# Performance work log

Hardware: AMD Instinct MI355X
Metric: run time of the kernel (lower is better)

Reference implementation:

```python
import jax, jax.numpy as jnp
import numpy as np

D_MODEL = 1024
N_HEADS = 16
D_K = D_MODEL // N_HEADS
D_FF = 4096
B, S = 4, 2048
EPS = 1e-5


def setup_inputs() -> dict:
    key = jax.random.key(0)
    ks = jax.random.split(key, 16)
    s = 0.02
    inp = {
        'x': jax.random.normal(ks[0], (B, S, D_MODEL), dtype=jnp.float32),
        'Wq': jax.random.normal(ks[1], (D_MODEL, D_MODEL), dtype=jnp.float32) * s,
        'bq': jnp.zeros((D_MODEL,), jnp.float32),
        'Wk': jax.random.normal(ks[2], (D_MODEL, D_MODEL), dtype=jnp.float32) * s,
        'bk': jnp.zeros((D_MODEL,), jnp.float32),
        'Wv': jax.random.normal(ks[3], (D_MODEL, D_MODEL), dtype=jnp.float32) * s,
        'bv': jnp.zeros((D_MODEL,), jnp.float32),
        'Wo': jax.random.normal(ks[4], (D_MODEL, D_MODEL), dtype=jnp.float32) * s,
        'bo': jnp.zeros((D_MODEL,), jnp.float32),
        'W1': jax.random.normal(ks[5], (D_MODEL, D_FF), dtype=jnp.float32) * s,
        'b1': jnp.zeros((D_FF,), jnp.float32),
        'W2': jax.random.normal(ks[6], (D_FF, D_MODEL), dtype=jnp.float32) * s,
        'b2': jnp.zeros((D_MODEL,), jnp.float32),
        'g1': jnp.ones((D_MODEL,), jnp.float32),
        'be1': jnp.zeros((D_MODEL,), jnp.float32),
        'g2': jnp.ones((D_MODEL,), jnp.float32),
        'be2': jnp.zeros((D_MODEL,), jnp.float32),
    }
    return inp


def _layernorm(x, g, b):
    mu = jnp.mean(x, axis=-1, keepdims=True)
    var = jnp.var(x, axis=-1, keepdims=True)
    return (x - mu) * jax.lax.rsqrt(var + EPS) * g + b


def reference(x, Wq, bq, Wk, bk, Wv, bv, Wo, bo, W1, b1, W2, b2, g1, be1, g2, be2):
    # Multi-head self-attention (mask=None, dropout in eval -> identity)
    q = (x @ Wq + bq).reshape(B, S, N_HEADS, D_K).transpose(0, 2, 1, 3)  # [B,H,S,Dk]
    k = (x @ Wk + bk).reshape(B, S, N_HEADS, D_K).transpose(0, 2, 1, 3)
    v = (x @ Wv + bv).reshape(B, S, N_HEADS, D_K).transpose(0, 2, 1, 3)
    scores = jnp.einsum('bhqd,bhkd->bhqk', q, k) / jnp.sqrt(jnp.float32(D_K))
    attn = jax.nn.softmax(scores, axis=-1)
    out = jnp.einsum('bhqk,bhkd->bhqd', attn, v)          # [B,H,S,Dk]
    out = out.transpose(0, 2, 1, 3).reshape(B, S, D_MODEL)
    att_out = out @ Wo + bo
    x2 = _layernorm(x + att_out, g1, be1)
    ff = jax.nn.relu(x2 @ W1 + b1) @ W2 + b2
    return _layernorm(x2 + ff, g2, be2)
```

## Files before the change

### kernel.cpp

```cpp
#include <hip/hip_runtime.h>
#include <hip/hip_bf16.h>

typedef __attribute__((ext_vector_type(8)))  __bf16 bf16x8;
typedef __attribute__((ext_vector_type(4)))  float  f32x4;
typedef __attribute__((ext_vector_type(16))) float  f32x16;

static __device__ __forceinline__ unsigned short f2bf(float x) {
    unsigned int u = __float_as_uint(x);
    unsigned int r = (u + 0x7FFFu + ((u >> 16) & 1u)) >> 16;
    return (unsigned short)r;
}
static __device__ __forceinline__ float bf2f(unsigned short u) {
    return __uint_as_float(((unsigned int)u) << 16);
}

static __device__ __forceinline__ float fast_exp2(float x) {
    float r;
    asm("v_exp_f32 %0, %1" : "=v"(r) : "v"(x));
    return r;
}
static __device__ __forceinline__ unsigned int cvt_pk_bf16(float a, float b) {
    unsigned int r;
    asm("v_cvt_pk_bf16_f32 %0, %1, %2" : "=v"(r) : "v"(a), "v"(b));
    return r;
}

static __device__ __forceinline__ void gload_lds16(const ushort* g, ushort* l) {
    __builtin_amdgcn_global_load_lds((const __attribute__((address_space(1))) void*)g,
                                     (__attribute__((address_space(3))) void*)l, 16, 0, 0);
}

static __device__ __forceinline__ void barrier_fence() {
    __builtin_amdgcn_s_barrier();
    __builtin_amdgcn_sched_barrier(0);
    asm volatile("" ::: "memory");
}

static __device__ __forceinline__ int xcd_swz(int id, int nwg) {
    return (id & 7) * (nwg >> 3) + (id >> 3);
}

__global__ __launch_bounds__(256) void cast_bf16_kernel(const float* __restrict__ in,
                                                        ushort* __restrict__ out, int n4) {
    int i = blockIdx.x * 256 + threadIdx.x;
    if (i < n4) {
        float4 v = reinterpret_cast<const float4*>(in)[i];
        ushort4 o;
        o.x = f2bf(v.x); o.y = f2bf(v.y); o.z = f2bf(v.z); o.w = f2bf(v.w);
        reinterpret_cast<ushort4*>(out)[i] = o;
    }
}

__global__ __launch_bounds__(256) void transpose_cast_kernel(const float* __restrict__ in,
                                                             ushort* __restrict__ out,
                                                             int K, int N) {
    __shared__ float tile[32][33];
    const int tx = threadIdx.x;
    const int ty = threadIdx.y;
    const int n0 = blockIdx.x * 32;
    const int k0 = blockIdx.y * 32;
    for (int i = ty; i < 32; i += 8)
        tile[i][tx] = in[(size_t)(k0 + i) * N + n0 + tx];
    __syncthreads();
    for (int i = ty; i < 32; i += 8)
        out[(size_t)(n0 + i) * K + k0 + tx] = f2bf(tile[tx][i]);
}

__global__ __launch_bounds__(256) void transpose_cast3_kernel(const float* __restrict__ w0,
                                                              const float* __restrict__ w1,
                                                              const float* __restrict__ w2,
                                                              ushort* __restrict__ out) {
    __shared__ float tile[32][33];
    const int tx = threadIdx.x;
    const int ty = threadIdx.y;
    const int n0 = blockIdx.x * 32;
    const int k0 = blockIdx.y * 32;
    const int z  = blockIdx.z;
    const float* in = (z == 0) ? w0 : (z == 1 ? w1 : w2);
    ushort* o = out + (size_t)z * 1024 * 1024;
    for (int i = ty; i < 32; i += 8)
        tile[i][tx] = in[(size_t)(k0 + i) * 1024 + n0 + tx];
    __syncthreads();
    for (int i = ty; i < 32; i += 8)
        o[(size_t)(n0 + i) * 1024 + k0 + tx] = f2bf(tile[tx][i]);
}

template<int RELU, int OUTBF, int QKV, int RES>
__global__ __launch_bounds__(256) void gemm_p3(const ushort* __restrict__ A,
                                               const ushort* __restrict__ Bt,
                                               const float* __restrict__ b0,
                                               const float* __restrict__ b1_,
                                               const float* __restrict__ b2_,
                                               const void* __restrict__ xres,
                                               void* __restrict__ Cp,
                                               int M, int N, int K) {
    __shared__ ushort As[3][4096];
    __shared__ ushort Bs[3][4096];
    const int tid  = threadIdx.x;
    const int lane = tid & 63;
    const int w    = tid >> 6;
    const int wr   = w >> 1, wc = w & 1;
    const int nwg = gridDim.x * gridDim.y;
    int wid = xcd_swz(blockIdx.y * gridDim.x + blockIdx.x, nwg);
    const int bx = wid % gridDim.x;
    const int by = wid / gridDim.x;
    const int m0 = by * 128;
    const int n0 = bx * 128;
    const int lr = lane & 15;
    const int lg = lane >> 4;
    const int xc = (lg ^ ((lr >> 1) & 3)) * 8;

    const int r0 = w * 32 + (lane >> 2);
    const int c8 = ((lane & 3) ^ ((lane >> 3) & 3)) * 8;
    const ushort* gA0 = A  + (size_t)(m0 + r0)      * K + c8;
    const ushort* gA1 = A  + (size_t)(m0 + r0 + 16) * K + c8;
    const ushort* gB0 = Bt + (size_t)(n0 + r0)      * K + c8;
    const ushort* gB1 = Bt + (size_t)(n0 + r0 + 16) * K + c8;
    const int wb = w * 1024;

    f32x4 acc[4][4];
    const f32x4 z = {0.f, 0.f, 0.f, 0.f};
#pragma unroll
    for (int i = 0; i < 4; i++)
#pragma unroll
        for (int j = 0; j < 4; j++) acc[i][j] = z;

    const int nt = K >> 5;

#pragma unroll
    for (int t = 0; t < 2; ++t) {
        const int kn = t * 32;
        gload_lds16(gA0 + kn, &As[t][wb]);
        gload_lds16(gA1 + kn, &As[t][wb + 512]);
        gload_lds16(gB0 + kn, &Bs[t][wb]);
        gload_lds16(gB1 + kn, &Bs[t][wb + 512]);
    }

    int cur = 0;
    for (int t = 0; t < nt; ++t) {
        if (t + 1 < nt) asm volatile("s_waitcnt vmcnt(4)" ::: "memory");
        else            asm volatile("s_waitcnt vmcnt(0)" ::: "memory");
        barrier_fence();

        if (t + 2 < nt) {
            const int bi = (cur + 2 >= 3) ? cur - 1 : cur + 2;
            const int kn = (t + 2) * 32;
            gload_lds16(gA0 + kn, &As[bi][wb]);
            gload_lds16(gA1 + kn, &As[bi][wb + 512]);
            gload_lds16(gB0 + kn, &Bs[bi][wb]);
            gload_lds16(gB1 + kn, &Bs[bi][wb + 512]);
        }

        const ushort* Asb = As[cur];
        const ushort* Bsb = Bs[cur];
        bf16x8 af[4], bfr[4];
#pragma unroll
        for (int i = 0; i < 4; i++)
            af[i] = *reinterpret_cast<const bf16x8*>(&Asb[(wr * 64 + i * 16 + lr) * 32 + xc]);
#pragma unroll
        for (int j = 0; j < 4; j++)
            bfr[j] = *reinterpret_cast<const bf16x8*>(&Bsb[(wc * 64 + j * 16 + lr) * 32 + xc]);
#pragma unroll
        for (int i = 0; i < 4; i++)
#pragma unroll
            for (int j = 0; j < 4; j++)
                acc[i][j] = __builtin_amdgcn_mfma_f32_16x16x32_bf16(af[i], bfr[j], acc[i][j], 0, 0, 0);

        cur = (cur == 2) ? 0 : cur + 1;
    }

    const float* bias;
    float qscale = 1.0f;
    if (QKV) {
        bias = (n0 < 1024) ? b0 : (n0 < 2048 ? b1_ : b2_);
        if (n0 < 1024) qscale = 0.18033688f;
    } else {
        bias = b0;
    }
    const int nb = QKV ? (n0 & 1023) : n0;
    const int rbase = (lane >> 4) * 4;
#pragma unroll
    for (int i = 0; i < 4; i++) {
#pragma unroll
        for (int j = 0; j < 4; j++) {
            const int cloc = wc * 64 + j * 16 + lr;
            const float bv = bias[nb + cloc];
#pragma unroll
            for (int r = 0; r < 4; r++) {
                const int row = m0 + wr * 64 + i * 16 + rbase + r;
                float v = acc[i][j][r] + bv;
                if (RES == 1) v += ((const float*)xres)[(size_t)row * N + n0 + cloc];
                if (RES == 2) v += bf2f(((const ushort*)xres)[(size_t)row * N + n0 + cloc]);
                if (RELU) v = v > 0.f ? v : 0.f;
                if (QKV)  v *= qscale;
                if (OUTBF) ((ushort*)Cp)[(size_t)row * N + n0 + cloc] = f2bf(v);
                else       ((float*)Cp)[(size_t)row * N + n0 + cloc] = v;
            }
        }
    }
}

template<int RELU, int OUTBF, int RES>
__global__ __launch_bounds__(256) void gemm_n64(const ushort* __restrict__ A,
                                                const ushort* __restrict__ Bt,
                                                const float* __restrict__ bias,
                                                const void* __restrict__ xres,
                                                void* __restrict__ Cp,
                                                int M, int N, int K) {
    __shared__ ushort As[3][4096];
    __shared__ ushort Bs[3][2048];
    const int tid  = threadIdx.x;
    const int lane = tid & 63;
    const int w    = tid >> 6;
    const int wr   = w >> 1, wc = w & 1;
    const int nwg = gridDim.x * gridDim.y;
    int wid = xcd_swz(blockIdx.y * gridDim.x + blockIdx.x, nwg);
    const int bx = wid % gridDim.x;
    const int by = wid / gridDim.x;
    const int m0 = by * 128;
    const int n0 = bx * 64;
    const int lr = lane & 15;
    const int lg = lane >> 4;
    const int xc = (lg ^ ((lr >> 1) & 3)) * 8;

    const int r0 = w * 32 + (lane >> 2);
    const int c8 = ((lane & 3) ^ ((lane >> 3) & 3)) * 8;
    const ushort* gA0 = A  + (size_t)(m0 + r0)      * K + c8;
    const ushort* gA1 = A  + (size_t)(m0 + r0 + 16) * K + c8;
    const ushort* gB0 = Bt + (size_t)(n0 + (tid >> 2)) * K + c8;
    const int wb  = w * 1024;
    const int wbB = w * 512;

    f32x4 acc[4][2];
    const f32x4 z = {0.f, 0.f, 0.f, 0.f};
#pragma unroll
    for (int i = 0; i < 4; i++)
#pragma unroll
        for (int j = 0; j < 2; j++) acc[i][j] = z;

    const int nt = K >> 5;

#pragma unroll
    for (int t = 0; t < 2; ++t) {
        const int kn = t * 32;
        gload_lds16(gA0 + kn, &As[t][wb]);
        gload_lds16(gA1 + kn, &As[t][wb + 512]);
        gload_lds16(gB0 + kn, &Bs[t][wbB]);
    }

    int cur = 0;
    for (int t = 0; t < nt; ++t) {
        if (t + 1 < nt) asm volatile("s_waitcnt vmcnt(3)" ::: "memory");
        else            asm volatile("s_waitcnt vmcnt(0)" ::: "memory");
        barrier_fence();

        if (t + 2 < nt) {
            const int bi = (cur + 2 >= 3) ? cur - 1 : cur + 2;
            const int kn = (t + 2) * 32;
            gload_lds16(gA0 + kn, &As[bi][wb]);
            gload_lds16(gA1 + kn, &As[bi][wb + 512]);
            gload_lds16(gB0 + kn, &Bs[bi][wbB]);
        }

        const ushort* Asb = As[cur];
        const ushort* Bsb = Bs[cur];
        bf16x8 af[4], bfr[2];
#pragma unroll
        for (int i = 0; i < 4; i++)
            af[i] = *reinterpret_cast<const bf16x8*>(&Asb[(wr * 64 + i * 16 + lr) * 32 + xc]);
#pragma unroll
        for (int j = 0; j < 2; j++)
            bfr[j] = *reinterpret_cast<const bf16x8*>(&Bsb[(wc * 32 + j * 16 + lr) * 32 + xc]);
#pragma unroll
        for (int i = 0; i < 4; i++)
#pragma unroll
            for (int j = 0; j < 2; j++)
                acc[i][j] = __builtin_amdgcn_mfma_f32_16x16x32_bf16(af[i], bfr[j], acc[i][j], 0, 0, 0);

        cur = (cur == 2) ? 0 : cur + 1;
    }

    const int rbase = (lane >> 4) * 4;
#pragma unroll
    for (int i = 0; i < 4; i++) {
#pragma unroll
        for (int j = 0; j < 2; j++) {
            const int cloc = wc * 32 + j * 16 + lr;
            const float bv = bias[n0 + cloc];
#pragma unroll
            for (int r = 0; r < 4; r++) {
                const int row = m0 + wr * 64 + i * 16 + rbase + r;
                float v = acc[i][j][r] + bv;
                if (RES == 1) v += ((const float*)xres)[(size_t)row * N + n0 + cloc];
                if (RES == 2) v += bf2f(((const ushort*)xres)[(size_t)row * N + n0 + cloc]);
                if (RELU) v = v > 0.f ? v : 0.f;
                if (OUTBF) ((ushort*)Cp)[(size_t)row * N + n0 + cloc] = f2bf(v);
                else       ((float*)Cp)[(size_t)row * N + n0 + cloc] = v;
            }
        }
    }
}

#define ASWZ(row, col) ((row) * 64 + ((col) ^ ((((row) ^ ((row) >> 3)) & 7) << 3)))

__global__ __launch_bounds__(256, 3) void attn_kernel(const ushort* __restrict__ QKV,
                                                      ushort* __restrict__ O) {
    __shared__ ushort Ks[2][4096];
    __shared__ ushort Vt[2][4096];
    const int tid  = threadIdx.x;
    const int lane = tid & 63;
    const int w    = tid >> 6;
    const int l31  = lane & 31;
    const int hi   = lane >> 5;

    int blk = xcd_swz(blockIdx.x, gridDim.x);
    const int qb = blk & 15;
    const int h  = (blk >> 4) & 15;
    const int b  = blk >> 8;
    const int s0 = qb * 128 + w * 32;
    const size_t rowb   = (size_t)b * 2048;
    const size_t base_q = rowb * 3072 + (size_t)h * 64;
    const size_t base_k = base_q + 1024;
    const size_t base_v = base_q + 2048;
    const size_t base_o = rowb * 1024 + (size_t)h * 64;

    bf16x8 qf[4];
#pragma unroll
    for (int ks = 0; ks < 4; ks++)
        qf[ks] = *reinterpret_cast<const bf16x8*>(
            &QKV[base_q + (size_t)(s0 + l31) * 3072 + ks * 16 + 8 * hi]);

    int off8[2][4];
#pragma unroll
    for (int sub = 0; sub < 2; sub++)
#pragma unroll
        for (int ks = 0; ks < 4; ks++)
            off8[sub][ks] = ASWZ(sub * 32 + l31, ks * 16 + 8 * hi);

    const int tS2 = tid >> 3;
    const int ccS = tid & 7;
    int voff[8];
#pragma unroll
    for (int jj = 0; jj < 8; jj++)
        voff[jj] = ASWZ(ccS * 8 + jj, 2 * tS2);
    const int tk1 = tS2 + 32;
    const int sz0 = (tS2 ^ (tS2 >> 3)) & 7;
    const int sz1 = (tk1 ^ (tk1 >> 3)) & 7;
    const ushort* pK0 = QKV + base_k + (size_t)tS2 * 3072 + (ccS ^ sz0) * 8;
    const ushort* pK1 = QKV + base_k + (size_t)tk1 * 3072 + (ccS ^ sz1) * 8;
    const ushort* pV0 = QKV + base_v + (size_t)(2 * tS2)     * 3072 + ccS * 8;
    const ushort* pV1 = QKV + base_v + (size_t)(2 * tS2 + 1) * 3072 + ccS * 8;
    const size_t step = (size_t)64 * 3072;

    gload_lds16(pK0, &Ks[0][w * 512]);
    gload_lds16(pK1, &Ks[0][2048 + w * 512]);
    {
        int4 v0 = *reinterpret_cast<const int4*>(pV0);
        int4 v1 = *reinterpret_cast<const int4*>(pV1);
        const ushort* vs0 = reinterpret_cast<const ushort*>(&v0);
        const ushort* vs1 = reinterpret_cast<const ushort*>(&v1);
#pragma unroll
        for (int jj = 0; jj < 8; jj++)
            *reinterpret_cast<unsigned*>(&Vt[0][voff[jj]]) =
                (unsigned)vs0[jj] | ((unsigned)vs1[jj] << 16);
    }
    pK0 += step; pK1 += step; pV0 += step; pV1 += step;
    __syncthreads();

    f32x16 oacc0, oacc1;
    for (int i = 0; i < 16; i++) { oacc0[i] = 0.f; oacc1[i] = 0.f; }
    float lacc = 0.f;
    int cur = 0;

    for (int it = 0; it < 32; ++it) {
        int4 nv0, nv1;
        if (it < 31) {
            gload_lds16(pK0, &Ks[cur ^ 1][w * 512]);
            gload_lds16(pK1, &Ks[cur ^ 1][2048 + w * 512]);
            nv0 = *reinterpret_cast<const int4*>(pV0);
            nv1 = *reinterpret_cast<const int4*>(pV1);
            pK0 += step; pK1 += step; pV0 += step; pV1 += step;
        }

        f32x16 sa0, sa1;
        for (int i = 0; i < 16; i++) { sa0[i] = 0.f; sa1[i] = 0.f; }
        __builtin_amdgcn_s_setprio(1);
#pragma unroll
        for (int ks = 0; ks < 4; ks++) {
            bf16x8 k0 = *reinterpret_cast<const bf16x8*>(&Ks[cur][off8[0][ks]]);
            sa0 = __builtin_amdgcn_mfma_f32_32x32x16_bf16(k0, qf[ks], sa0, 0, 0, 0);
        }
#pragma unroll
        for (int ks = 0; ks < 4; ks++) {
            bf16x8 k1 = *reinterpret_cast<const bf16x8*>(&Ks[cur][off8[1][ks]]);
            sa1 = __builtin_amdgcn_mfma_f32_32x32x16_bf16(k1, qf[ks], sa1, 0, 0, 0);
        }
        __builtin_amdgcn_s_setprio(0);

        unsigned pk0[8], pk1[8];
#pragma unroll
        for (int i = 0; i < 8; i++) {
            float plo = fast_exp2(sa0[2 * i]);
            float phi = fast_exp2(sa0[2 * i + 1]);
            lacc += plo + phi;
            pk0[i] = cvt_pk_bf16(plo, phi);
        }
#pragma unroll
        for (int i = 0; i < 8; i++) {
            float plo = fast_exp2(sa1[2 * i]);
            float phi = fast_exp2(sa1[2 * i + 1]);
            lacc += plo + phi;
            pk1[i] = cvt_pk_bf16(plo, phi);
        }

        __builtin_amdgcn_s_setprio(1);
#pragma unroll
        for (int ks = 0; ks < 4; ks++) {
            const int bi = 4 * (ks & 1);
            unsigned a, bb, c, d;
            if (ks < 2) { a = pk0[bi]; bb = pk0[bi + 1]; c = pk0[bi + 2]; d = pk0[bi + 3]; }
            else        { a = pk1[bi]; bb = pk1[bi + 1]; c = pk1[bi + 2]; d = pk1[bi + 3]; }
            asm("v_permlane32_swap_b32 %0, %1" : "+v"(a), "+v"(c));
            asm("v_permlane32_swap_b32 %0, %1" : "+v"(bb), "+v"(d));
            union { unsigned u[4]; bf16x8 v; } fr;
            fr.u[0] = a; fr.u[1] = bb; fr.u[2] = c; fr.u[3] = d;
            bf16x8 v0 = *reinterpret_cast<const bf16x8*>(&Vt[cur][off8[0][ks]]);
            oacc0 = __builtin_amdgcn_mfma_f32_32x32x16_bf16(fr.v, v0, oacc0, 0, 0, 0);
            bf16x8 v1 = *reinterpret_cast<const bf16x8*>(&Vt[cur][off8[1][ks]]);
            oacc1 = __builtin_amdgcn_mfma_f32_32x32x16_bf16(fr.v, v1, oacc1, 0, 0, 0);
        }
        __builtin_amdgcn_s_setprio(0);

        if (it < 31) {
            const ushort* vs0 = reinterpret_cast<const ushort*>(&nv0);
            const ushort* vs1 = reinterpret_cast<const ushort*>(&nv1);
#pragma unroll
            for (int jj = 0; jj < 8; jj++)
                *reinterpret_cast<unsigned*>(&Vt[cur ^ 1][voff[jj]]) =
                    (unsigned)vs0[jj] | ((unsigned)vs1[jj] << 16);
        }
        __syncthreads();
        cur ^= 1;
    }

    const float ltot = lacc + __shfl_xor(lacc, 32);
    const float inv  = 1.f / ltot;
#pragma unroll
    for (int r = 0; r < 16; r++) {
        const int qloc = (r & 3) + 8 * (r >> 2) + 4 * hi;
        const float invq = __shfl(inv, qloc);
        const size_t rowoff = base_o + (size_t)(s0 + qloc) * 1024 + l31;
        O[rowoff]      = f2bf(oacc0[r] * invq);
        O[rowoff + 32] = f2bf(oacc1[r] * invq);
    }
}

template<int OUTBF>
__global__ __launch_bounds__(256) void ln_one(const ushort* __restrict__ zin,
                                              const float* __restrict__ g,
                                              const float* __restrict__ be,
                                              void* __restrict__ out) {
    const int row = blockIdx.x;
    const int tid = threadIdx.x;
    const ushort4 zv = reinterpret_cast<const ushort4*>(zin + (size_t)row * 1024)[tid];
    float v[4] = {bf2f(zv.x), bf2f(zv.y), bf2f(zv.z), bf2f(zv.w)};
    float s  = v[0] + v[1] + v[2] + v[3];
    float s2 = v[0]*v[0] + v[1]*v[1] + v[2]*v[2] + v[3]*v[3];
    for (int off = 32; off; off >>= 1) { s += __shfl_down(s, off); s2 += __shfl_down(s2, off); }
    __shared__ float red[8];
    const int w = tid >> 6, lane = tid & 63;
    if (lane == 0) { red[w] = s; red[4 + w] = s2; }
    __syncthreads();
    if (tid == 0) {
        const float ts  = red[0] + red[1] + red[2] + red[3];
        const float ts2 = red[4] + red[5] + red[6] + red[7];
        const float mu  = ts * (1.f / 1024.f);
        const float var = ts2 * (1.f / 1024.f) - mu * mu;
        red[0] = mu;
        red[1] = rsqrtf(var + 1e-5f);
    }
    __syncthreads();
    const float mu = red[0], rs = red[1];
    const float4 gv = reinterpret_cast<const float4*>(g)[tid];
    const float4 bv = reinterpret_cast<const float4*>(be)[tid];
    float o0 = (v[0] - mu) * rs * gv.x + bv.x;
    float o1 = (v[1] - mu) * rs * gv.y + bv.y;
    float o2 = (v[2] - mu) * rs * gv.z + bv.z;
    float o3 = (v[3] - mu) * rs * gv.w + bv.w;
    if (OUTBF) {
        ushort4 ob;
        ob.x = f2bf(o0); ob.y = f2bf(o1); ob.z = f2bf(o2); ob.w = f2bf(o3);
        reinterpret_cast<ushort4*>((ushort*)out + (size_t)row * 1024)[tid] = ob;
    } else {
        float4 of;
        of.x = o0; of.y = o1; of.z = o2; of.w = o3;
        reinterpret_cast<float4*>((float*)out + (size_t)row * 1024)[tid] = of;
    }
}

extern "C" void kernel_launch(void* const* d_in, const int* in_sizes, int n_in,
                              void* d_out, int out_size, void* d_ws, size_t ws_size,
                              hipStream_t stream) {
    const float* x  = (const float*)d_in[0];
    const float* Wq = (const float*)d_in[1];  const float* bq = (const float*)d_in[2];
    const float* Wk = (const float*)d_in[3];  const float* bk = (const float*)d_in[4];
    const float* Wv = (const float*)d_in[5];  const float* bv = (const float*)d_in[6];
    const float* Wo = (const float*)d_in[7];  const float* bo = (const float*)d_in[8];
    const float* W1 = (const float*)d_in[9];  const float* b1 = (const float*)d_in[10];
    const float* W2 = (const float*)d_in[11]; const float* b2 = (const float*)d_in[12];
    const float* g1 = (const float*)d_in[13]; const float* be1 = (const float*)d_in[14];
    const float* g2 = (const float*)d_in[15]; const float* be2 = (const float*)d_in[16];

    char* ws = (char*)d_ws;
    const size_t MBy = (size_t)1 << 20;
    ushort* xb    = (ushort*)(ws + 0 * MBy);
    ushort* wqkvT = (ushort*)(ws + 16 * MBy);
    ushort* woT   = (ushort*)(ws + 22 * MBy);
    ushort* w1T   = (ushort*)(ws + 24 * MBy);
    ushort* w2T   = (ushort*)(ws + 32 * MBy);
    ushort* QKVb  = (ushort*)(ws + 40 * MBy);
    ushort* AOb   = (ushort*)(ws + 88 * MBy);
    ushort* h1    = (ushort*)(ws + 40 * MBy);
    ushort* z1b   = (ushort*)(ws + 104 * MBy);
    ushort* z2b   = (ushort*)(ws + 104 * MBy);
    ushort* x2b   = (ushort*)(ws + 120 * MBy);
    (void)ws_size; (void)n_in; (void)in_sizes; (void)out_size;

    const int M = 8192;

    cast_bf16_kernel<<<(M * 1024 / 4 + 255) / 256, 256, 0, stream>>>(x, xb, M * 1024 / 4);
    dim3 tb(32, 8);
    transpose_cast3_kernel<<<dim3(32, 32, 3), tb, 0, stream>>>(Wq, Wk, Wv, wqkvT);
    transpose_cast_kernel<<<dim3(32, 32),  tb, 0, stream>>>(Wo, woT, 1024, 1024);
    transpose_cast_kernel<<<dim3(128, 32), tb, 0, stream>>>(W1, w1T, 1024, 4096);
    transpose_cast_kernel<<<dim3(32, 128), tb, 0, stream>>>(W2, w2T, 4096, 1024);

    gemm_p3<0, 1, 1, 0><<<dim3(24, 64), 256, 0, stream>>>(xb, wqkvT, bq, bk, bv, nullptr,
                                                          QKVb, M, 3072, 1024);

    attn_kernel<<<1024, 256, 0, stream>>>(QKVb, AOb);

    gemm_n64<0, 1, 1><<<dim3(16, 64), 256, 0, stream>>>(AOb, woT, bo, x, z1b,
                                                        M, 1024, 1024);

    ln_one<1><<<M, 256, 0, stream>>>(z1b, g1, be1, x2b);

    gemm_p3<1, 1, 0, 0><<<dim3(32, 64), 256, 0, stream>>>(x2b, w1T, b1, nullptr, nullptr,
                                                          nullptr, h1, M, 4096, 1024);
    gemm_n64<0, 1, 2><<<dim3(16, 64), 256, 0, stream>>>(h1, w2T, b2, x2b, z2b,
                                                        M, 1024, 4096);

    ln_one<0><<<M, 256, 0, stream>>>(z2b, g2, be2, (float*)d_out);
}
```

Before: 419.8 us.

## Split-K the FFN down-projection with 128x128 tiles and fuse reduction into LayerNorm

The W2 GEMM changes from 128x64 tiles over the full K=4096 to 128x128 tiles split into two K halves. Each half writes bf16 partials, and a new LayerNorm kernel sums them with the residual and bias. The Wo projection now uses the wider gemm_p3 kernel instead of gemm_n64, and the attention kernel's launch bound asks for 4 blocks per CU instead of 3. The goal is better data reuse and occupancy, at the cost of extra partial-sum traffic, bf16 rounding of the partials, and possible register pressure in attention.

Result: no change. 419.6 us (-0.0%).

```diff
diff --git a/kernel.cpp b/kernel.cpp
--- a/kernel.cpp
+++ b/kernel.cpp
@@ -200,57 +200,57 @@
     }
 }
 
-template<int RELU, int OUTBF, int RES>
-__global__ __launch_bounds__(256) void gemm_n64(const ushort* __restrict__ A,
-                                                const ushort* __restrict__ Bt,
-                                                const float* __restrict__ bias,
-                                                const void* __restrict__ xres,
-                                                void* __restrict__ Cp,
-                                                int M, int N, int K) {
+__global__ __launch_bounds__(256) void gemm_sk(const ushort* __restrict__ A,
+                                               const ushort* __restrict__ Bt,
+                                               ushort* __restrict__ P,
+                                               int M, int N, int ld, int Khalf) {
     __shared__ ushort As[3][4096];
-    __shared__ ushort Bs[3][2048];
+    __shared__ ushort Bs[3][4096];
     const int tid  = threadIdx.x;
     const int lane = tid & 63;
     const int w    = tid >> 6;
     const int wr   = w >> 1, wc = w & 1;
     const int nwg = gridDim.x * gridDim.y;
     int wid = xcd_swz(blockIdx.y * gridDim.x + blockIdx.x, nwg);
-    const int bx = wid % gridDim.x;
-    const int by = wid / gridDim.x;
-    const int m0 = by * 128;
-    const int n0 = bx * 64;
+    const int bx  = wid % gridDim.x;
+    const int byz = wid / gridDim.x;
+    const int m0  = (byz & 63) * 128;
+    const int sk  = byz >> 6;
+    const int koff = sk * Khalf;
+    const int n0  = bx * 128;
     const int lr = lane & 15;
     const int lg = lane >> 4;
     const int xc = (lg ^ ((lr >> 1) & 3)) * 8;
 
     const int r0 = w * 32 + (lane >> 2);
     const int c8 = ((lane & 3) ^ ((lane >> 3) & 3)) * 8;
-    const ushort* gA0 = A  + (size_t)(m0 + r0)      * K + c8;
-    const ushort* gA1 = A  + (size_t)(m0 + r0 + 16) * K + c8;
-    const ushort* gB0 = Bt + (size_t)(n0 + (tid >> 2)) * K + c8;
-    const int wb  = w * 1024;
-    const int wbB = w * 512;
-
-    f32x4 acc[4][2];
+    const ushort* gA0 = A  + (size_t)(m0 + r0)      * ld + koff + c8;
+    const ushort* gA1 = A  + (size_t)(m0 + r0 + 16) * ld + koff + c8;
+    const ushort* gB0 = Bt + (size_t)(n0 + r0)      * ld + koff + c8;
+    const ushort* gB1 = Bt + (size_t)(n0 + r0 + 16) * ld + koff + c8;
+    const int wb = w * 1024;
+
+    f32x4 acc[4][4];
     const f32x4 z = {0.f, 0.f, 0.f, 0.f};
 #pragma unroll
     for (int i = 0; i < 4; i++)
 #pragma unroll
-        for (int j = 0; j < 2; j++) acc[i][j] = z;
-
-    const int nt = K >> 5;
+        for (int j = 0; j < 4; j++) acc[i][j] = z;
+
+    const int nt = Khalf >> 5;
 
 #pragma unroll
     for (int t = 0; t < 2; ++t) {
         const int kn = t * 32;
         gload_lds16(gA0 + kn, &As[t][wb]);
         gload_lds16(gA1 + kn, &As[t][wb + 512]);
-        gload_lds16(gB0 + kn, &Bs[t][wbB]);
+        gload_lds16(gB0 + kn, &Bs[t][wb]);
+        gload_lds16(gB1 + kn, &Bs[t][wb + 512]);
     }
 
     int cur = 0;
     for (int t = 0; t < nt; ++t) {
-        if (t + 1 < nt) asm volatile("s_waitcnt vmcnt(3)" ::: "memory");
+        if (t + 1 < nt) asm volatile("s_waitcnt vmcnt(4)" ::: "memory");
         else            asm volatile("s_waitcnt vmcnt(0)" ::: "memory");
         barrier_fence();
 
@@ -259,43 +259,39 @@
             const int kn = (t + 2) * 32;
             gload_lds16(gA0 + kn, &As[bi][wb]);
             gload_lds16(gA1 + kn, &As[bi][wb + 512]);
-            gload_lds16(gB0 + kn, &Bs[bi][wbB]);
+            gload_lds16(gB0 + kn, &Bs[bi][wb]);
+            gload_lds16(gB1 + kn, &Bs[bi][wb + 512]);
         }
 
         const ushort* Asb = As[cur];
         const ushort* Bsb = Bs[cur];
-        bf16x8 af[4], bfr[2];
+        bf16x8 af[4], bfr[4];
 #pragma unroll
         for (int i = 0; i < 4; i++)
             af[i] = *reinterpret_cast<const bf16x8*>(&Asb[(wr * 64 + i * 16 + lr) * 32 + xc]);
 #pragma unroll
-        for (int j = 0; j < 2; j++)
-            bfr[j] = *reinterpret_cast<const bf16x8*>(&Bsb[(wc * 32 + j * 16 + lr) * 32 + xc]);
+        for (int j = 0; j < 4; j++)
+            bfr[j] = *reinterpret_cast<const bf16x8*>(&Bsb[(wc * 64 + j * 16 + lr) * 32 + xc]);
 #pragma unroll
         for (int i = 0; i < 4; i++)
 #pragma unroll
-            for (int j = 0; j < 2; j++)
+            for (int j = 0; j < 4; j++)
                 acc[i][j] = __builtin_amdgcn_mfma_f32_16x16x32_bf16(af[i], bfr[j], acc[i][j], 0, 0, 0);
 
         cur = (cur == 2) ? 0 : cur + 1;
     }
 
+    ushort* Pp = P + (size_t)sk * M * N;
     const int rbase = (lane >> 4) * 4;
 #pragma unroll
     for (int i = 0; i < 4; i++) {
 #pragma unroll
-        for (int j = 0; j < 2; j++) {
-            const int cloc = wc * 32 + j * 16 + lr;
-            const float bv = bias[n0 + cloc];
+        for (int j = 0; j < 4; j++) {
+            const int cloc = wc * 64 + j * 16 + lr;
 #pragma unroll
             for (int r = 0; r < 4; r++) {
                 const int row = m0 + wr * 64 + i * 16 + rbase + r;
-                float v = acc[i][j][r] + bv;
-                if (RES == 1) v += ((const float*)xres)[(size_t)row * N + n0 + cloc];
-                if (RES == 2) v += bf2f(((const ushort*)xres)[(size_t)row * N + n0 + cloc]);
-                if (RELU) v = v > 0.f ? v : 0.f;
-                if (OUTBF) ((ushort*)Cp)[(size_t)row * N + n0 + cloc] = f2bf(v);
-                else       ((float*)Cp)[(size_t)row * N + n0 + cloc] = v;
+                Pp[(size_t)row * N + n0 + cloc] = f2bf(acc[i][j][r]);
             }
         }
     }
@@ -303,7 +299,7 @@
 
 #define ASWZ(row, col) ((row) * 64 + ((col) ^ ((((row) ^ ((row) >> 3)) & 7) << 3)))
 
-__global__ __launch_bounds__(256, 3) void attn_kernel(const ushort* __restrict__ QKV,
+__global__ __launch_bounds__(256, 4) void attn_kernel(const ushort* __restrict__ QKV,
                                                       ushort* __restrict__ O) {
     __shared__ ushort Ks[2][4096];
     __shared__ ushort Vt[2][4096];
@@ -455,11 +451,10 @@
     }
 }
 
-template<int OUTBF>
-__global__ __launch_bounds__(256) void ln_one(const ushort* __restrict__ zin,
-                                              const float* __restrict__ g,
-                                              const float* __restrict__ be,
-                                              void* __restrict__ out) {
+__global__ __launch_bounds__(256) void ln_one_b(const ushort* __restrict__ zin,
+                                                const float* __restrict__ g,
+                                                const float* __restrict__ be,
+                                                ushort* __restrict__ out) {
     const int row = blockIdx.x;
     const int tid = threadIdx.x;
     const ushort4 zv = reinterpret_cast<const ushort4*>(zin + (size_t)row * 1024)[tid];
@@ -483,19 +478,58 @@
     const float mu = red[0], rs = red[1];
     const float4 gv = reinterpret_cast<const float4*>(g)[tid];
     const float4 bv = reinterpret_cast<const float4*>(be)[tid];
-    float o0 = (v[0] - mu) * rs * gv.x + bv.x;
-    float o1 = (v[1] - mu) * rs * gv.y + bv.y;
-    float o2 = (v[2] - mu) * rs * gv.z + bv.z;
-    float o3 = (v[3] - mu) * rs * gv.w + bv.w;
-    if (OUTBF) {
-        ushort4 ob;
-        ob.x = f2bf(o0); ob.y = f2bf(o1); ob.z = f2bf(o2); ob.w = f2bf(o3);
-        reinterpret_cast<ushort4*>((ushort*)out + (size_t)row * 1024)[tid] = ob;
-    } else {
-        float4 of;
-        of.x = o0; of.y = o1; of.z = o2; of.w = o3;
-        reinterpret_cast<float4*>((float*)out + (size_t)row * 1024)[tid] = of;
-    }
+    ushort4 ob;
+    ob.x = f2bf((v[0] - mu) * rs * gv.x + bv.x);
+    ob.y = f2bf((v[1] - mu) * rs * gv.y + bv.y);
+    ob.z = f2bf((v[2] - mu) * rs * gv.z + bv.z);
+    ob.w = f2bf((v[3] - mu) * rs * gv.w + bv.w);
+    reinterpret_cast<ushort4*>(out + (size_t)row * 1024)[tid] = ob;
+}
+
+__global__ __launch_bounds__(256) void ln2_reduce(const ushort* __restrict__ x2,
+                                                  const ushort* __restrict__ p0,
+                                                  const ushort* __restrict__ p1,
+                                                  const float* __restrict__ b2,
+                                                  const float* __restrict__ g,
+                                                  const float* __restrict__ be,
+                                                  float* __restrict__ out) {
+    const int row = blockIdx.x;
+    const int tid = threadIdx.x;
+    const size_t off = (size_t)row * 1024;
+    const ushort4 xv = reinterpret_cast<const ushort4*>(x2 + off)[tid];
+    const ushort4 q0 = reinterpret_cast<const ushort4*>(p0 + off)[tid];
+    const ushort4 q1 = reinterpret_cast<const ushort4*>(p1 + off)[tid];
+    const float4 bb = reinterpret_cast<const float4*>(b2)[tid];
+    float v[4];
+    v[0] = bf2f(xv.x) + bf2f(q0.x) + bf2f(q1.x) + bb.x;
+    v[1] = bf2f(xv.y) + bf2f(q0.y) + bf2f(q1.y) + bb.y;
+    v[2] = bf2f(xv.z) + bf2f(q0.z) + bf2f(q1.z) + bb.z;
+    v[3] = bf2f(xv.w) + bf2f(q0.w) + bf2f(q1.w) + bb.w;
+    float s  = v[0] + v[1] + v[2] + v[3];
+    float s2 = v[0]*v[0] + v[1]*v[1] + v[2]*v[2] + v[3]*v[3];
+    for (int o = 32; o; o >>= 1) { s += __shfl_down(s, o); s2 += __shfl_down(s2, o); }
+    __shared__ float red[8];
+    const int w = tid >> 6, lane = tid & 63;
+    if (lane == 0) { red[w] = s; red[4 + w] = s2; }
+    __syncthreads();
+    if (tid == 0) {
+        const float ts  = red[0] + red[1] + red[2] + red[3];
+        const float ts2 = red[4] + red[5] + red[6] + red[7];
+        const float mu  = ts * (1.f / 1024.f);
+        const float var = ts2 * (1.f / 1024.f) - mu * mu;
+        red[0] = mu;
+        red[1] = rsqrtf(var + 1e-5f);
+    }
+    __syncthreads();
+    const float mu = red[0], rs = red[1];
+    const float4 gv = reinterpret_cast<const float4*>(g)[tid];
+    const float4 bv = reinterpret_cast<const float4*>(be)[tid];
+    float4 of;
+    of.x = (v[0] - mu) * rs * gv.x + bv.x;
+    of.y = (v[1] - mu) * rs * gv.y + bv.y;
+    of.z = (v[2] - mu) * rs * gv.z + bv.z;
+    of.w = (v[3] - mu) * rs * gv.w + bv.w;
+    reinterpret_cast<float4*>(out + off)[tid] = of;
 }
 
 extern "C" void kernel_launch(void* const* d_in, const int* in_sizes, int n_in,
@@ -522,8 +556,8 @@
     ushort* AOb   = (ushort*)(ws + 88 * MBy);
     ushort* h1    = (ushort*)(ws + 40 * MBy);
     ushort* z1b   = (ushort*)(ws + 104 * MBy);
-    ushort* z2b   = (ushort*)(ws + 104 * MBy);
     ushort* x2b   = (ushort*)(ws + 120 * MBy);
+    ushort* psk   = (ushort*)(ws + 136 * MBy);
     (void)ws_size; (void)n_in; (void)in_sizes; (void)out_size;
 
     const int M = 8192;
@@ -540,15 +574,16 @@
 
     attn_kernel<<<1024, 256, 0, stream>>>(QKVb, AOb);
 
-    gemm_n64<0, 1, 1><<<dim3(16, 64), 256, 0, stream>>>(AOb, woT, bo, x, z1b,
-                                                        M, 1024, 1024);
-
-    ln_one<1><<<M, 256, 0, stream>>>(z1b, g1, be1, x2b);
+    gemm_p3<0, 1, 0, 1><<<dim3(8, 64), 256, 0, stream>>>(AOb, woT, bo, nullptr, nullptr, x,
+                                                         z1b, M, 1024, 1024);
+
+    ln_one_b<<<M, 256, 0, stream>>>(z1b, g1, be1, x2b);
 
     gemm_p3<1, 1, 0, 0><<<dim3(32, 64), 256, 0, stream>>>(x2b, w1T, b1, nullptr, nullptr,
                                                           nullptr, h1, M, 4096, 1024);
-    gemm_n64<0, 1, 2><<<dim3(16, 64), 256, 0, stream>>>(h1, w2T, b2, x2b, z2b,
-                                                        M, 1024, 4096);
-
-    ln_one<0><<<M, 256, 0, stream>>>(z2b, g2, be2, (float*)d_out);
-}
+
+    gemm_sk<<<dim3(8, 128), 256, 0, stream>>>(h1, w2T, psk, M, 1024, 4096, 2048);
+
+    ln2_reduce<<<M, 256, 0, stream>>>(x2b, psk, psk + (size_t)M * 1024, b2, g2, be2,
+                                      (float*)d_out);
+}
```
